# Performance work log

Hardware: AMD Instinct MI355X
Metric: run time of the kernel (lower is better)

Reference implementation:

```python
import jax, jax.numpy as jnp
import numpy as np

B, S, D, H, O = 8192, 64, 128, 128, 128  # sets, max set size, input_dim, hidden_dim, out_dim


def setup_inputs() -> dict:
    key = jax.random.key(0)
    ks = jax.random.split(key, 10)
    neigh = jax.random.normal(ks[0], (B, S, D), dtype=jnp.float32)
    lengths = jax.random.randint(ks[1], (B,), 1, S + 1)  # each set has >= 1 neighbor

    def lin_w(k, fan_in, fan_out):
        return jax.random.normal(k, (fan_in, fan_out), dtype=jnp.float32) / np.sqrt(fan_in)

    Wq = lin_w(ks[2], D, H); bq = jax.random.normal(ks[3], (H,), dtype=jnp.float32) * 0.01
    Wk = lin_w(ks[4], D, H); bk = jax.random.normal(ks[5], (H,), dtype=jnp.float32) * 0.01
    Wv = lin_w(ks[6], D, H); bv = jax.random.normal(ks[7], (H,), dtype=jnp.float32) * 0.01
    Wo = lin_w(ks[8], H, O); bo = jax.random.normal(ks[9], (O,), dtype=jnp.float32) * 0.01
    return dict(neigh=neigh, lengths=lengths, Wq=Wq, bq=bq, Wk=Wk, bk=bk,
                Wv=Wv, bv=bv, Wo=Wo, bo=bo)


def reference(neigh, lengths, Wq, bq, Wk, bk, Wv, bv, Wo, bo):
    # neigh: [B, S, D] padded ragged sets; lengths: [B] valid neighbor counts.
    q = neigh @ Wq + bq                                   # [B, S, H]
    k = neigh @ Wk + bk                                   # [B, S, H]
    v = neigh @ Wv + bv                                   # [B, S, H]
    # Original divides by sqrt(input_dim) (not hidden_dim) -- kept faithful.
    scores = jnp.einsum('bsh,bth->bst', q, k) / jnp.sqrt(jnp.asarray(D, q.dtype))
    valid = jnp.arange(S)[None, :] < lengths[:, None]     # [B, S] key/row validity
    scores = jnp.where(valid[:, None, :], scores, jnp.finfo(scores.dtype).min)
    attn = jax.nn.softmax(scores, axis=-1)                # [B, S, S]
    atten_out = jnp.einsum('bst,bth->bsh', attn, v)       # [B, S, H]
    o = atten_out @ Wo + bo                               # [B, S, O]
    # Mean-pool over valid rows of each set (torch.mean over dim 0 per set).
    m = valid[:, :, None].astype(o.dtype)
    pooled = jnp.sum(o * m, axis=1) / lengths[:, None].astype(o.dtype)
    return pooled                                         # [B, O]
```

## Files before the change

kernel.cpp:

```cpp
#include <hip/hip_runtime.h>
#include <hip/hip_bf16.h>
#include <cstdint>


typedef __attribute__((ext_vector_type(8))) short bf16x8;
typedef __attribute__((ext_vector_type(4))) float f32x4;

__device__ __forceinline__ unsigned short f2bf(float f) {
    unsigned int u = __builtin_bit_cast(unsigned int, f);
    u += 0x7fffu + ((u >> 16) & 1u);
    return (unsigned short)(u >> 16);
}
__device__ __forceinline__ float bf2f(unsigned short s) {
    unsigned int u = ((unsigned int)s) << 16;
    return __builtin_bit_cast(float, u);
}
__device__ __forceinline__ unsigned cvt_pk_bf16(float lo, float hi) {
    unsigned r;
    asm("v_cvt_pk_bf16_f32 %0, %1, %2" : "=v"(r) : "v"(lo), "v"(hi));
    return r;
}

__global__ __launch_bounds__(256) void setformer_pre(
    const float* __restrict__ Wq, const float* __restrict__ Wk,
    const float* __restrict__ Wv, const float* __restrict__ Wo,
    const float* __restrict__ bq, const float* __restrict__ bv,
    const float* __restrict__ bo,
    unsigned short* __restrict__ MtBf, float* __restrict__ Nmat,
    float* __restrict__ wsv, float* __restrict__ cvec)
{
    __shared__ float sKd[128], sVd[128];
    const int d = blockIdx.x, tid = threadIdx.x;
    if (tid < 128) { sKd[tid] = Wk[d*128 + tid]; sVd[tid] = Wv[d*128 + tid]; }
    __syncthreads();
    const float invs = 0.088388347648318447f;
    if (tid < 128) {
        const int e = tid;
        float acc = 0.f;
        for (int h = 0; h < 128; ++h) acc = fmaf(Wq[e*128 + h], sKd[h], acc);
        MtBf[d*128 + e] = f2bf(acc * invs);
    } else {
        const int o = tid - 128;
        float acc = 0.f;
        for (int h = 0; h < 128; ++h) acc = fmaf(sVd[h], Wo[h*128 + o], acc);
        Nmat[d*128 + o] = acc;
    }
    if (d == 0 && tid < 128) {
        float a = 0.f, c = 0.f;
        for (int h = 0; h < 128; ++h) {
            a = fmaf(Wk[tid*128 + h], bq[h], a);
            c = fmaf(bv[h], Wo[h*128 + tid], c);
        }
        wsv[tid]  = a * invs;
        cvec[tid] = c + bo[tid];
    }
}

__global__ __launch_bounds__(512, 6) void setformer_main(
    const float* __restrict__ neigh, const int* __restrict__ lengths,
    const unsigned short* __restrict__ MtBf,
    const float* __restrict__ wsv, float* __restrict__ yout)
{
    __shared__ unsigned short sX[64 * 128];
    __shared__ unsigned short sG[64 * 128];
    __shared__ float sWp[4][64];
    __shared__ float sW[64];
    __shared__ float sY4[4][128];

    const int tid  = threadIdx.x;
    const int lane = tid & 63;
    const int wv   = tid >> 6;
    const int l15  = lane & 15;
    const int lg   = lane >> 4;
    const int b    = blockIdx.x;

    const char* bB = (const char*)MtBf + (wv*16 + l15) * 256;
    bf16x8 bfr0 = *(const bf16x8*)(bB +   0 + lg*16);
    bf16x8 bfr1 = *(const bf16x8*)(bB +  64 + lg*16);
    bf16x8 bfr2 = *(const bf16x8*)(bB + 128 + lg*16);
    bf16x8 bfr3 = *(const bf16x8*)(bB + 192 + lg*16);
    const float wadd = wsv[wv*16 + l15];

    const float4* np4 = (const float4*)(neigh + (size_t)b * (64 * 128));
    const float4 fA = np4[tid];

    int L = lengths[b];
    L = max(1, min(64, L));
    const int ST = (L + 15) >> 4;

    if (tid < 256) ((float*)sWp)[tid] = 0.f;

    {
        const int r = tid >> 5, c4 = tid & 31;
        uint2 val;
        if (r < L) { val.x = cvt_pk_bf16(fA.x, fA.y); val.y = cvt_pk_bf16(fA.z, fA.w); }
        else       { val.x = 0u; val.y = 0u; }
        *(uint2*)((char*)sX + r*256 + ((c4*8) ^ ((r & 7) << 4))) = val;
    }
    {
        const int nCh = ST * 16 * 32;
        for (int idx = 512 + tid; idx < nCh; idx += 512) {
            const int r = idx >> 5, c4 = idx & 31;
            uint2 val = {0u, 0u};
            if (r < L) {
                float4 f = np4[idx];
                val.x = cvt_pk_bf16(f.x, f.y);
                val.y = cvt_pk_bf16(f.z, f.w);
            }
            *(uint2*)((char*)sX + r*256 + ((c4*8) ^ ((r & 7) << 4))) = val;
        }
    }
    __syncthreads();

    for (int st = 0; st < ST; ++st) {
        const char* aB = (const char*)sX + (st*16 + l15) * 256;
        f32x4 acc = {0.f, 0.f, 0.f, 0.f};
        bf16x8 a0 = *(const bf16x8*)(aB + ((  0 + lg*16) ^ ((l15 & 7) << 4)));
        acc = __builtin_amdgcn_mfma_f32_16x16x32_bf16(a0, bfr0, acc, 0, 0, 0);
        bf16x8 a1 = *(const bf16x8*)(aB + (( 64 + lg*16) ^ ((l15 & 7) << 4)));
        acc = __builtin_amdgcn_mfma_f32_16x16x32_bf16(a1, bfr1, acc, 0, 0, 0);
        bf16x8 a2 = *(const bf16x8*)(aB + ((128 + lg*16) ^ ((l15 & 7) << 4)));
        acc = __builtin_amdgcn_mfma_f32_16x16x32_bf16(a2, bfr2, acc, 0, 0, 0);
        bf16x8 a3 = *(const bf16x8*)(aB + ((192 + lg*16) ^ ((l15 & 7) << 4)));
        acc = __builtin_amdgcn_mfma_f32_16x16x32_bf16(a3, bfr3, acc, 0, 0, 0);
        #pragma unroll
        for (int j = 0; j < 4; ++j) {
            const int gr  = st*16 + lg*4 + j;
            const int gcb = ((wv*16 + l15) * 2) ^ ((gr & 7) << 4);
            const float g = acc[j] + wadd;
            *(unsigned short*)((char*)sG + gr*256 + gcb) =
                (unsigned short)cvt_pk_bf16(g, g);
        }
    }
    __syncthreads();

    if (wv < ST) {
        const char* aB = (const char*)sG + (wv*16 + l15) * 256;
        bf16x8 afr[4];
        #pragma unroll
        for (int kk = 0; kk < 4; ++kk)
            afr[kk] = *(const bf16x8*)(aB + ((kk*64 + lg*16) ^ ((l15 & 7) << 4)));

        f32x4 sc[4];
        #pragma unroll
        for (int tt = 0; tt < 4; ++tt) {
            f32x4 acc = {0.f, 0.f, 0.f, 0.f};
            if (tt < ST) {
                const char* bBt = (const char*)sX + (tt*16 + l15) * 256;
                #pragma unroll
                for (int kk = 0; kk < 4; ++kk) {
                    bf16x8 bfr = *(const bf16x8*)(bBt + ((kk*64 + lg*16) ^ ((l15 & 7) << 4)));
                    acc = __builtin_amdgcn_mfma_f32_16x16x32_bf16(afr[kk], bfr, acc, 0, 0, 0);
                }
            }
            sc[tt] = acc;
        }

        float den[4] = {0.f, 0.f, 0.f, 0.f};
        #pragma unroll
        for (int tt = 0; tt < 4; ++tt) {
            if (tt < ST) {
                const bool tv = (tt*16 + l15) < L;
                #pragma unroll
                for (int j = 0; j < 4; ++j) {
                    float p = tv ? __expf(sc[tt][j]) : 0.f;
                    sc[tt][j] = p;
                    den[j] += p;
                }
            }
        }
        #pragma unroll
        for (int j = 0; j < 4; ++j) {
            #pragma unroll
            for (int off = 1; off < 16; off <<= 1)
                den[j] += __shfl_xor(den[j], off);
        }
        const float invL = 1.0f / (float)L;
        float rinv[4];
        #pragma unroll
        for (int j = 0; j < 4; ++j) {
            const int srow = wv*16 + lg*4 + j;
            rinv[j] = (srow < L) ? (invL / den[j]) : 0.f;
        }
        #pragma unroll
        for (int tt = 0; tt < 4; ++tt) {
            if (tt < ST) {
                float cp = sc[tt][0]*rinv[0] + sc[tt][1]*rinv[1]
                         + sc[tt][2]*rinv[2] + sc[tt][3]*rinv[3];
                cp += __shfl_xor(cp, 16);
                cp += __shfl_xor(cp, 32);
                if (lane < 16) sWp[wv][tt*16 + lane] = cp;
            }
        }
    }
    __syncthreads();

    if (tid < 64)
        sW[tid] = sWp[0][tid] + sWp[1][tid] + sWp[2][tid] + sWp[3][tid];
    __syncthreads();

    {
        const int q = tid >> 7, col = tid & 127;
        float acc = 0.f;
        const int t0 = q * 16, t1 = min(t0 + 16, L);
        for (int t = t0; t < t1; ++t) {
            const unsigned short xv = *(const unsigned short*)
                ((const char*)sX + t*256 + ((col*2) ^ ((t & 7) << 4)));
            acc = fmaf(sW[t], bf2f(xv), acc);
        }
        sY4[q][col] = acc;
    }
    __syncthreads();

    if (tid < 128)
        yout[(size_t)b*128 + tid] = sY4[0][tid] + sY4[1][tid]
                                  + sY4[2][tid] + sY4[3][tid];
}

__global__ __launch_bounds__(256) void setformer_out(
    const float* __restrict__ yin, const float* __restrict__ Nmat,
    const float* __restrict__ cvec, float* __restrict__ out)
{
    __shared__ float sy[16 * 128];
    const int tid = threadIdx.x;
    const size_t r0 = (size_t)blockIdx.x * 16;
    const float4* y4 = (const float4*)(yin + r0 * 128);
    float4* sy4 = (float4*)sy;
    sy4[tid]       = y4[tid];
    sy4[tid + 256] = y4[tid + 256];
    __syncthreads();
    const int col = tid & 127;
    const int rg  = (tid >> 7) * 8;
    float acc[8];
    #pragma unroll
    for (int i = 0; i < 8; ++i) acc[i] = 0.f;
    for (int d = 0; d < 128; d += 2) {
        const float n0 = Nmat[(d+0)*128 + col];
        const float n1 = Nmat[(d+1)*128 + col];
        #pragma unroll
        for (int i = 0; i < 8; ++i) {
            const float2 yv = *(const float2*)&sy[(rg + i)*128 + d];
            acc[i] = fmaf(yv.x, n0, acc[i]);
            acc[i] = fmaf(yv.y, n1, acc[i]);
        }
    }
    const float c = cvec[col];
    #pragma unroll
    for (int i = 0; i < 8; ++i)
        out[(r0 + rg + i)*128 + col] = acc[i] + c;
}

extern "C" void kernel_launch(void* const* d_in, const int* in_sizes, int n_in,
                              void* d_out, int out_size, void* d_ws, size_t ws_size,
                              hipStream_t stream)
{
    const float* neigh   = (const float*)d_in[0];
    const int*   lengths = (const int*)  d_in[1];
    const float* Wq = (const float*)d_in[2];
    const float* bq = (const float*)d_in[3];
    const float* Wk = (const float*)d_in[4];
    const float* Wv = (const float*)d_in[6];
    const float* bv = (const float*)d_in[7];
    const float* Wo = (const float*)d_in[8];
    const float* bo = (const float*)d_in[9];

    const int B = in_sizes[1];

    char* ws = (char*)d_ws;
    unsigned short* MtBf = (unsigned short*)(ws);
    float* Nmat = (float*)(ws + 32768);
    float* wsv  = (float*)(ws + 32768 + 65536);
    float* cvec = (float*)(ws + 32768 + 65536 + 512);
    float* ybuf = (float*)(ws + 32768 + 65536 + 1024);

    hipLaunchKernelGGL(setformer_pre, dim3(128), dim3(256), 0, stream,
                       Wq, Wk, Wv, Wo, bq, bv, bo, MtBf, Nmat, wsv, cvec);
    hipLaunchKernelGGL(setformer_main, dim3(B), dim3(512), 0, stream,
                       neigh, lengths, MtBf, wsv, ybuf);
    hipLaunchKernelGGL(setformer_out, dim3(B / 16), dim3(256), 0, stream,
                       ybuf, Nmat, cvec, (float*)d_out);
}
```

Baseline: 83.31 us.

## Process four sets per block with register-prefetched double-buffered LDS staging

The main kernel now loops over four sets per block (grid reduced by four), which amortises the per-block load of the projection fragments. While the current set's G matrix is computed, the next set's neighbour rows are prefetched into registers and later written into a second LDS buffer. The per-wave partial arrays are replaced by shared-memory atomic adds into sW and sY. The cost is extra LDS (a second X buffer), more registers, fewer blocks to hide latency, and additional barriers per set.

```diff
diff --git a/kernel.cpp b/kernel.cpp
--- a/kernel.cpp
+++ b/kernel.cpp
@@ -56,16 +56,18 @@
     }
 }
 
+#define NSETS 4
+
 __global__ __launch_bounds__(512, 6) void setformer_main(
     const float* __restrict__ neigh, const int* __restrict__ lengths,
     const unsigned short* __restrict__ MtBf,
     const float* __restrict__ wsv, float* __restrict__ yout)
 {
-    __shared__ unsigned short sX[64 * 128];
+    __shared__ unsigned short sXa[64 * 128];
+    __shared__ unsigned short sXb[64 * 128];
     __shared__ unsigned short sG[64 * 128];
-    __shared__ float sWp[4][64];
     __shared__ float sW[64];
-    __shared__ float sY4[4][128];
+    __shared__ float sY[128];
 
     const int tid  = threadIdx.x;
     const int lane = tid & 63;
@@ -73,6 +75,7 @@
     const int l15  = lane & 15;
     const int lg   = lane >> 4;
     const int b    = blockIdx.x;
+    const int GD   = gridDim.x;
 
     const char* bB = (const char*)MtBf + (wv*16 + l15) * 256;
     bf16x8 bfr0 = *(const bf16x8*)(bB +   0 + lg*16);
@@ -81,140 +84,171 @@
     bf16x8 bfr3 = *(const bf16x8*)(bB + 192 + lg*16);
     const float wadd = wsv[wv*16 + l15];
 
-    const float4* np4 = (const float4*)(neigh + (size_t)b * (64 * 128));
-    const float4 fA = np4[tid];
-
-    int L = lengths[b];
-    L = max(1, min(64, L));
-    const int ST = (L + 15) >> 4;
-
-    if (tid < 256) ((float*)sWp)[tid] = 0.f;
+    if (tid < 64) sW[tid] = 0.f;
+    else if (tid < 192) sY[tid - 64] = 0.f;
 
     {
-        const int r = tid >> 5, c4 = tid & 31;
-        uint2 val;
-        if (r < L) { val.x = cvt_pk_bf16(fA.x, fA.y); val.y = cvt_pk_bf16(fA.z, fA.w); }
-        else       { val.x = 0u; val.y = 0u; }
-        *(uint2*)((char*)sX + r*256 + ((c4*8) ^ ((r & 7) << 4))) = val;
-    }
-    {
-        const int nCh = ST * 16 * 32;
-        for (int idx = 512 + tid; idx < nCh; idx += 512) {
-            const int r = idx >> 5, c4 = idx & 31;
-            uint2 val = {0u, 0u};
-            if (r < L) {
-                float4 f = np4[idx];
-                val.x = cvt_pk_bf16(f.x, f.y);
-                val.y = cvt_pk_bf16(f.z, f.w);
-            }
-            *(uint2*)((char*)sX + r*256 + ((c4*8) ^ ((r & 7) << 4))) = val;
+        int L0 = lengths[b]; L0 = max(1, min(64, L0));
+        const float4* np4 = (const float4*)(neigh + (size_t)b * 8192);
+        #pragma unroll
+        for (int i = 0; i < 4; ++i) {
+            if (i*16 < L0) {
+                const int idx = tid + i*512, r = idx >> 5, c4 = idx & 31;
+                uint2 v = {0u, 0u};
+                if (r < L0) {
+                    float4 f = np4[idx];
+                    v.x = cvt_pk_bf16(f.x, f.y);
+                    v.y = cvt_pk_bf16(f.z, f.w);
+                }
+                *(uint2*)((char*)sXa + r*256 + ((c4*8) ^ ((r & 7) << 4))) = v;
+            }
         }
     }
     __syncthreads();
 
-    for (int st = 0; st < ST; ++st) {
-        const char* aB = (const char*)sX + (st*16 + l15) * 256;
-        f32x4 acc = {0.f, 0.f, 0.f, 0.f};
-        bf16x8 a0 = *(const bf16x8*)(aB + ((  0 + lg*16) ^ ((l15 & 7) << 4)));
-        acc = __builtin_amdgcn_mfma_f32_16x16x32_bf16(a0, bfr0, acc, 0, 0, 0);
-        bf16x8 a1 = *(const bf16x8*)(aB + (( 64 + lg*16) ^ ((l15 & 7) << 4)));
-        acc = __builtin_amdgcn_mfma_f32_16x16x32_bf16(a1, bfr1, acc, 0, 0, 0);
-        bf16x8 a2 = *(const bf16x8*)(aB + ((128 + lg*16) ^ ((l15 & 7) << 4)));
-        acc = __builtin_amdgcn_mfma_f32_16x16x32_bf16(a2, bfr2, acc, 0, 0, 0);
-        bf16x8 a3 = *(const bf16x8*)(aB + ((192 + lg*16) ^ ((l15 & 7) << 4)));
-        acc = __builtin_amdgcn_mfma_f32_16x16x32_bf16(a3, bfr3, acc, 0, 0, 0);
-        #pragma unroll
-        for (int j = 0; j < 4; ++j) {
-            const int gr  = st*16 + lg*4 + j;
-            const int gcb = ((wv*16 + l15) * 2) ^ ((gr & 7) << 4);
-            const float g = acc[j] + wadd;
-            *(unsigned short*)((char*)sG + gr*256 + gcb) =
-                (unsigned short)cvt_pk_bf16(g, g);
-        }
-    }
-    __syncthreads();
-
-    if (wv < ST) {
-        const char* aB = (const char*)sG + (wv*16 + l15) * 256;
-        bf16x8 afr[4];
-        #pragma unroll
-        for (int kk = 0; kk < 4; ++kk)
-            afr[kk] = *(const bf16x8*)(aB + ((kk*64 + lg*16) ^ ((l15 & 7) << 4)));
-
-        f32x4 sc[4];
-        #pragma unroll
-        for (int tt = 0; tt < 4; ++tt) {
+    unsigned short* cur = sXa;
+    unsigned short* nxt = sXb;
+
+    for (int k = 0; k < NSETS; ++k) {
+        int L = lengths[b + k*GD]; L = max(1, min(64, L));
+        const int ST = (L + 15) >> 4;
+
+        float4 pf0 = {0,0,0,0}, pf1 = {0,0,0,0}, pf2 = {0,0,0,0}, pf3 = {0,0,0,0};
+        int Ln = 0;
+        if (k + 1 < NSETS) {
+            Ln = lengths[b + (k+1)*GD]; Ln = max(1, min(64, Ln));
+            const float4* np4n = (const float4*)(neigh + (size_t)(b + (k+1)*GD) * 8192);
+            { const int r = tid >> 5;          if (r < Ln) pf0 = np4n[tid];        }
+            { const int r = (tid + 512) >> 5;  if (r < Ln) pf1 = np4n[tid + 512];  }
+            { const int r = (tid + 1024) >> 5; if (r < Ln) pf2 = np4n[tid + 1024]; }
+            { const int r = (tid + 1536) >> 5; if (r < Ln) pf3 = np4n[tid + 1536]; }
+        }
+
+        for (int st = 0; st < ST; ++st) {
+            const char* aB = (const char*)cur + (st*16 + l15) * 256;
             f32x4 acc = {0.f, 0.f, 0.f, 0.f};
-            if (tt < ST) {
-                const char* bBt = (const char*)sX + (tt*16 + l15) * 256;
+            bf16x8 a0 = *(const bf16x8*)(aB + ((  0 + lg*16) ^ ((l15 & 7) << 4)));
+            acc = __builtin_amdgcn_mfma_f32_16x16x32_bf16(a0, bfr0, acc, 0, 0, 0);
+            bf16x8 a1 = *(const bf16x8*)(aB + (( 64 + lg*16) ^ ((l15 & 7) << 4)));
+            acc = __builtin_amdgcn_mfma_f32_16x16x32_bf16(a1, bfr1, acc, 0, 0, 0);
+            bf16x8 a2 = *(const bf16x8*)(aB + ((128 + lg*16) ^ ((l15 & 7) << 4)));
+            acc = __builtin_amdgcn_mfma_f32_16x16x32_bf16(a2, bfr2, acc, 0, 0, 0);
+            bf16x8 a3 = *(const bf16x8*)(aB + ((192 + lg*16) ^ ((l15 & 7) << 4)));
+            acc = __builtin_amdgcn_mfma_f32_16x16x32_bf16(a3, bfr3, acc, 0, 0, 0);
+            #pragma unroll
+            for (int j = 0; j < 4; ++j) {
+                const int gr  = st*16 + lg*4 + j;
+                const int gcb = ((wv*16 + l15) * 2) ^ ((gr & 7) << 4);
+                const float g = acc[j] + wadd;
+                *(unsigned short*)((char*)sG + gr*256 + gcb) =
+                    (unsigned short)cvt_pk_bf16(g, g);
+            }
+        }
+
+        if (k + 1 < NSETS) {
+            #pragma unroll
+            for (int i = 0; i < 4; ++i) {
+                if (i*16 < Ln) {
+                    const int idx = tid + i*512, r = idx >> 5, c4 = idx & 31;
+                    uint2 v = {0u, 0u};
+                    if (r < Ln) {
+                        const float4 f = (i == 0) ? pf0 : (i == 1) ? pf1
+                                       : (i == 2) ? pf2 : pf3;
+                        v.x = cvt_pk_bf16(f.x, f.y);
+                        v.y = cvt_pk_bf16(f.z, f.w);
+                    }
+                    *(uint2*)((char*)nxt + r*256 + ((c4*8) ^ ((r & 7) << 4))) = v;
+                }
+            }
+        }
+        __syncthreads();
+
+        if (wv < ST) {
+            const char* aB = (const char*)sG + (wv*16 + l15) * 256;
+            bf16x8 afr[4];
+            #pragma unroll
+            for (int kk = 0; kk < 4; ++kk)
+                afr[kk] = *(const bf16x8*)(aB + ((kk*64 + lg*16) ^ ((l15 & 7) << 4)));
+
+            f32x4 sc[4];
+            #pragma unroll
+            for (int tt = 0; tt < 4; ++tt) {
+                f32x4 acc = {0.f, 0.f, 0.f, 0.f};
+                if (tt < ST) {
+                    const char* bBt = (const char*)cur + (tt*16 + l15) * 256;
+                    #pragma unroll
+                    for (int kk = 0; kk < 4; ++kk) {
+                        bf16x8 bfr = *(const bf16x8*)(bBt + ((kk*64 + lg*16) ^ ((l15 & 7) << 4)));
+                        acc = __builtin_amdgcn_mfma_f32_16x16x32_bf16(afr[kk], bfr, acc, 0, 0, 0);
+                    }
+                }
+                sc[tt] = acc;
+            }
+
+            float den[4] = {0.f, 0.f, 0.f, 0.f};
+            #pragma unroll
+            for (int tt = 0; tt < 4; ++tt) {
+                if (tt < ST) {
+                    const bool tv = (tt*16 + l15) < L;
+                    #pragma unroll
+                    for (int j = 0; j < 4; ++j) {
+                        float p = tv ? __expf(sc[tt][j]) : 0.f;
+                        sc[tt][j] = p;
+                        den[j] += p;
+                    }
+                }
+            }
+            #pragma unroll
+            for (int j = 0; j < 4; ++j) {
                 #pragma unroll
-                for (int kk = 0; kk < 4; ++kk) {
-                    bf16x8 bfr = *(const bf16x8*)(bBt + ((kk*64 + lg*16) ^ ((l15 & 7) << 4)));
-                    acc = __builtin_amdgcn_mfma_f32_16x16x32_bf16(afr[kk], bfr, acc, 0, 0, 0);
-                }
-            }
-            sc[tt] = acc;
-        }
-
-        float den[4] = {0.f, 0.f, 0.f, 0.f};
-        #pragma unroll
-        for (int tt = 0; tt < 4; ++tt) {
-            if (tt < ST) {
-                const bool tv = (tt*16 + l15) < L;
-                #pragma unroll
-                for (int j = 0; j < 4; ++j) {
-                    float p = tv ? __expf(sc[tt][j]) : 0.f;
-                    sc[tt][j] = p;
-                    den[j] += p;
-                }
-            }
-        }
-        #pragma unroll
-        for (int j = 0; j < 4; ++j) {
-            #pragma unroll
-            for (int off = 1; off < 16; off <<= 1)
-                den[j] += __shfl_xor(den[j], off);
-        }
-        const float invL = 1.0f / (float)L;
-        float rinv[4];
-        #pragma unroll
-        for (int j = 0; j < 4; ++j) {
-            const int srow = wv*16 + lg*4 + j;
-            rinv[j] = (srow < L) ? (invL / den[j]) : 0.f;
-        }
-        #pragma unroll
-        for (int tt = 0; tt < 4; ++tt) {
-            if (tt < ST) {
-                float cp = sc[tt][0]*rinv[0] + sc[tt][1]*rinv[1]
-                         + sc[tt][2]*rinv[2] + sc[tt][3]*rinv[3];
-                cp += __shfl_xor(cp, 16);
-                cp += __shfl_xor(cp, 32);
-                if (lane < 16) sWp[wv][tt*16 + lane] = cp;
-            }
-        }
-    }
-    __syncthreads();
-
-    if (tid < 64)
-        sW[tid] = sWp[0][tid] + sWp[1][tid] + sWp[2][tid] + sWp[3][tid];
-    __syncthreads();
-
-    {
-        const int q = tid >> 7, col = tid & 127;
-        float acc = 0.f;
-        const int t0 = q * 16, t1 = min(t0 + 16, L);
-        for (int t = t0; t < t1; ++t) {
-            const unsigned short xv = *(const unsigned short*)
-                ((const char*)sX + t*256 + ((col*2) ^ ((t & 7) << 4)));
-            acc = fmaf(sW[t], bf2f(xv), acc);
-        }
-        sY4[q][col] = acc;
-    }
-    __syncthreads();
-
-    if (tid < 128)
-        yout[(size_t)b*128 + tid] = sY4[0][tid] + sY4[1][tid]
-                                  + sY4[2][tid] + sY4[3][tid];
+                for (int off = 1; off < 16; off <<= 1)
+                    den[j] += __shfl_xor(den[j], off);
+            }
+            const float invL = 1.0f / (float)L;
+            float rinv[4];
+            #pragma unroll
+            for (int j = 0; j < 4; ++j) {
+                const int srow = wv*16 + lg*4 + j;
+                rinv[j] = (srow < L) ? (invL / den[j]) : 0.f;
+            }
+            #pragma unroll
+            for (int tt = 0; tt < 4; ++tt) {
+                if (tt < ST) {
+                    float cp = sc[tt][0]*rinv[0] + sc[tt][1]*rinv[1]
+                             + sc[tt][2]*rinv[2] + sc[tt][3]*rinv[3];
+                    cp += __shfl_xor(cp, 16);
+                    cp += __shfl_xor(cp, 32);
+                    if (lane < 16) atomicAdd(&sW[tt*16 + lane], cp);
+                }
+            }
+        }
+        __syncthreads();
+
+        {
+            const int q = tid >> 7, col = tid & 127;
+            const int t0 = q * 16, t1 = min(t0 + 16, L);
+            if (t0 < L) {
+                float acc = 0.f;
+                for (int t = t0; t < t1; ++t) {
+                    const unsigned short xv = *(const unsigned short*)
+                        ((const char*)cur + t*256 + ((col*2) ^ ((t & 7) << 4)));
+                    acc = fmaf(sW[t], bf2f(xv), acc);
+                }
+                atomicAdd(&sY[col], acc);
+            }
+        }
+        __syncthreads();
+
+        if (tid < 128) {
+            yout[(size_t)(b + k*GD)*128 + tid] = sY[tid];
+            sY[tid] = 0.f;
+        } else if (tid < 192) {
+            sW[tid - 128] = 0.f;
+        }
+        __syncthreads();
+
+        unsigned short* t = cur; cur = nxt; nxt = t;
+    }
 }
 
 __global__ __launch_bounds__(256) void setformer_out(
@@ -275,7 +309,7 @@
 
     hipLaunchKernelGGL(setformer_pre, dim3(128), dim3(256), 0, stream,
                        Wq, Wk, Wv, Wo, bq, bv, bo, MtBf, Nmat, wsv, cvec);
-    hipLaunchKernelGGL(setformer_main, dim3(B), dim3(512), 0, stream,
+    hipLaunchKernelGGL(setformer_main, dim3(B / NSETS), dim3(512), 0, stream,
                        neigh, lengths, MtBf, wsv, ybuf);
     hipLaunchKernelGGL(setformer_out, dim3(B / 16), dim3(256), 0, stream,
                        ybuf, Nmat, cvec, (float*)d_out);
```

Measured after the change: 121.2 us. 45.5% more time.
